# Optimization experiments

Measured on AMD Instinct MI355X. Metric: run time of the kernel, lower is better.

The kernel has to match this reference:

```python
import jax, jax.numpy as jnp
import numpy as np

B, S, H = 2, 2048, 4096
NH, NKV, HD = 32, 8, 128
RD = 64  # partial rotary dim = head_dim * partial_rotary_factor
THETA = 10000.0


def setup_inputs() -> dict:
    key = jax.random.key(0)
    ks = jax.random.split(key, 6)
    hidden_states = jax.random.normal(ks[0], (B, S, H), dtype=jnp.float32)
    wq = jax.random.normal(ks[1], (H, NH * HD), dtype=jnp.float32) * 0.02
    wk = jax.random.normal(ks[2], (H, NKV * HD), dtype=jnp.float32) * 0.02
    wv = jax.random.normal(ks[3], (H, NKV * HD), dtype=jnp.float32) * 0.02
    wo = jax.random.normal(ks[4], (NH * HD, H), dtype=jnp.float32) * 0.02
    # default RoPE over rotary_dim=RD: inv_freq has RD//2 entries, emb = cat(freqs, freqs)
    inv_freq = 1.0 / (THETA ** (jnp.arange(0, RD, 2, dtype=jnp.float32) / RD))  # [RD//2]
    pos = jnp.arange(S, dtype=jnp.float32)
    freqs = pos[:, None] * inv_freq[None, :]               # [S, RD//2]
    emb = jnp.concatenate([freqs, freqs], axis=-1)          # [S, RD]
    cos = jnp.broadcast_to(jnp.cos(emb)[None], (B, S, RD))
    sin = jnp.broadcast_to(jnp.sin(emb)[None], (B, S, RD))
    return {"hidden_states": hidden_states, "wq": wq, "wk": wk, "wv": wv, "wo": wo,
            "cos": cos, "sin": sin}


def _rotate_half_interleaved(x):
    # GLM-style interleaved rotate: pairs (x0,x1) -> (-x1,x0)
    x1 = x[..., 0::2]
    x2 = x[..., 1::2]
    return jnp.stack((-x2, x1), axis=-1).reshape(x.shape)


def _apply_partial_rope(x, cos_i, sin_i):
    x_rot, x_pass = x[..., :RD], x[..., RD:]
    x_rot = x_rot * cos_i + _rotate_half_interleaved(x_rot) * sin_i
    return jnp.concatenate([x_rot, x_pass], axis=-1)


def reference(hidden_states, wq, wk, wv, wo, cos, sin):
    b, s, _ = hidden_states.shape
    # projections -> [B, nheads, S, head_dim]
    q = (hidden_states @ wq).reshape(b, s, NH, HD).transpose(0, 2, 1, 3)
    k = (hidden_states @ wk).reshape(b, s, NKV, HD).transpose(0, 2, 1, 3)
    v = (hidden_states @ wv).reshape(b, s, NKV, HD).transpose(0, 2, 1, 3)
    # GLM partial rotary: take first half of cos/sin and repeat-interleave by 2
    cos_i = jnp.repeat(cos[..., : RD // 2], 2, axis=-1)[:, None]  # [B,1,S,RD]
    sin_i = jnp.repeat(sin[..., : RD // 2], 2, axis=-1)[:, None]
    q = _apply_partial_rope(q, cos_i, sin_i)
    k = _apply_partial_rope(k, cos_i, sin_i)
    # repeat_kv for GQA
    rep = NH // NKV
    k = jnp.repeat(k, rep, axis=1)
    v = jnp.repeat(v, rep, axis=1)
    # causal SDPA, scaling = head_dim**-0.5
    scores = jnp.einsum('bhqd,bhkd->bhqk', q, k) * (HD ** -0.5)
    causal = jnp.tril(jnp.ones((s, s), dtype=bool))
    scores = jnp.where(causal[None, None], scores, jnp.finfo(scores.dtype).min)
    probs = jax.nn.softmax(scores, axis=-1)
    out = jnp.einsum('bhqk,bhkd->bhqd', probs, v)
    out = out.transpose(0, 2, 1, 3).reshape(b, s, NH * HD)
    return out @ wo
```

## Files before the change

### kernel.cpp

```cpp
#include <hip/hip_runtime.h>


typedef _Float16 f16;
typedef _Float16 f16x8 __attribute__((ext_vector_type(8)));
typedef float f32x4 __attribute__((ext_vector_type(4)));
typedef float f32x16 __attribute__((ext_vector_type(16)));

static constexpr int Bn = 2, Sn = 2048, Hn = 4096, NH = 32, NKV = 8, HD = 128;
static constexpr float QSC = 0.08838834764831845f * 1.44269504088896340736f;

#define AS1 __attribute__((address_space(1)))
#define AS3 __attribute__((address_space(3)))

__device__ __forceinline__ void async_ld16(const void* g, void* l) {
    __builtin_amdgcn_global_load_lds((const AS1 void*)g, (AS3 void*)l, 16, 0, 0);
}

__device__ __forceinline__ unsigned pk2(float a, float b) {
    unsigned r;
    asm("v_cvt_pkrtz_f16_f32 %0, %1, %2" : "=v"(r) : "v"(a), "v"(b));
    return r;
}

__device__ __forceinline__ float fexp2(float x) {
    float r;
    asm("v_exp_f32 %0, %1" : "=v"(r) : "v"(x));
    return r;
}

__global__ __launch_bounds__(256) void k_prep(
    const float* __restrict__ hs, f16* __restrict__ hid,
    const float* __restrict__ wq, const float* __restrict__ wk,
    const float* __restrict__ wv, const float* __restrict__ wo,
    f16* __restrict__ wqkv_t, f16* __restrict__ wo_t) {
    int bid = blockIdx.x;
    if (bid < 8192) {
        long i = ((long)bid * 256 + threadIdx.x) * 8;
        float4 a = *(const float4*)(hs + i);
        float4 b = *(const float4*)(hs + i + 4);
        f16x8 o = {(f16)a.x, (f16)a.y, (f16)a.z, (f16)a.w,
                   (f16)b.x, (f16)b.y, (f16)b.z, (f16)b.w};
        *(f16x8*)(hid + i) = o;
        return;
    }
    bid -= 8192;
    const float* src;
    f16* dst;
    int N, bx, by;
    if (bid < 4096)      { src = wq; dst = wqkv_t;                    N = 4096; bx = bid & 63; by = bid >> 6; }
    else if (bid < 5120) { bid -= 4096; src = wk; dst = wqkv_t + (long)4096 * 4096; N = 1024; bx = bid & 15; by = bid >> 4; }
    else if (bid < 6144) { bid -= 5120; src = wv; dst = wqkv_t + (long)5120 * 4096; N = 1024; bx = bid & 15; by = bid >> 4; }
    else                 { bid -= 6144; src = wo; dst = wo_t;         N = 4096; bx = bid & 63; by = bid >> 6; }
    __shared__ float tile[64][65];
    const int k0 = by * 64, n0 = bx * 64;
    const int tx = threadIdx.x & 63, ty = threadIdx.x >> 6;
#pragma unroll
    for (int r = ty; r < 64; r += 4)
        tile[r][tx] = src[(long)(k0 + r) * N + (n0 + tx)];
    __syncthreads();
#pragma unroll
    for (int r = ty; r < 64; r += 4)
        dst[(long)(n0 + r) * 4096 + (k0 + tx)] = (f16)tile[tx][r];
}

__device__ __forceinline__ void gemm256_core(
    const f16* __restrict__ A, const f16* __restrict__ Bt,
    char* L, int m0, int n0, f32x4 acc[8][4]) {
    const int t = threadIdx.x, lane = t & 63, wave = t >> 6;
    const int wm = wave >> 2, wn = wave & 3;
    const int fr = lane & 15, fg = lane >> 4;

    const int srowL = wave * 8 + (lane >> 3);
    const int scol  = 8 * ((lane & 7) ^ (lane >> 3));
    const f16* ga = A  + (long)(m0 + srowL) * 4096 + scol;
    const f16* gb = Bt + (long)(n0 + srowL) * 4096 + scol;
    const int woff = wave * 1024;

    auto ST = [&](int sel, int c, int row0, int kt) {
        const f16* g = sel ? gb : ga;
        async_ld16(g + (long)row0 * 4096 + kt * 64,
                   L + c * 65536 + sel * 32768 + row0 * 128 + woff);
    };

    ST(0, 0, 0, 0);   ST(0, 0, 64, 0);  ST(0, 0, 128, 0); ST(0, 0, 192, 0);
    ST(1, 0, 0, 0);   ST(1, 0, 64, 0);  ST(1, 0, 128, 0); ST(1, 0, 192, 0);
    ST(1, 1, 0, 1);   ST(1, 1, 64, 1);  ST(1, 1, 128, 1); ST(1, 1, 192, 1);
    ST(0, 1, 0, 1);   ST(0, 1, 128, 1);
    asm volatile("s_waitcnt vmcnt(6)" ::: "memory");
    __builtin_amdgcn_s_barrier();

    const int abase = wm * 128;
    const int bbase = wn * 64;

    for (int tt = 0; tt < 64; ++tt) {
        const int c = tt & 1;
        const char* bufA = L + c * 65536;
        const char* bufB = bufA + 32768;
        f16x8 bf[2][4];

#pragma unroll
        for (int q = 0; q < 4; ++q) {
            if (q == 0) {
#pragma unroll
                for (int ks = 0; ks < 2; ++ks)
#pragma unroll
                    for (int nf = 0; nf < 4; ++nf) {
                        int r = bbase + nf * 16 + fr;
                        bf[ks][nf] = *(const f16x8*)(bufB + r * 128 +
                                        ((ks * 64 + 16 * fg) ^ ((r & 7) << 4)));
                    }
            }
            f16x8 af[2][2];
#pragma unroll
            for (int ks = 0; ks < 2; ++ks)
#pragma unroll
                for (int i = 0; i < 2; ++i) {
                    int r = abase + (2 * q + i) * 16 + fr;
                    af[ks][i] = *(const f16x8*)(bufA + r * 128 +
                                    ((ks * 64 + 16 * fg) ^ ((r & 7) << 4)));
                }
            if (q == 0) { if (tt + 1 < 64) { ST(0, c ^ 1,  64, tt + 1);
                                             ST(0, c ^ 1, 192, tt + 1); } }
            if (q == 1) { if (tt + 2 < 64) { ST(1, c,   0, tt + 2);
                                             ST(1, c,  64, tt + 2); } }
            if (q == 2) { if (tt + 2 < 64) { ST(1, c, 128, tt + 2);
                                             ST(1, c, 192, tt + 2); } }
            if (q == 3) { if (tt + 2 < 64) { ST(0, c,   0, tt + 2);
                                             ST(0, c, 128, tt + 2); } }
            __builtin_amdgcn_s_barrier();
            __builtin_amdgcn_s_setprio(1);
#pragma unroll
            for (int ks = 0; ks < 2; ++ks)
#pragma unroll
                for (int i = 0; i < 2; ++i)
#pragma unroll
                    for (int nf = 0; nf < 4; ++nf)
                        acc[2 * q + i][nf] = __builtin_amdgcn_mfma_f32_16x16x32_f16(
                            af[ks][i], bf[ks][nf], acc[2 * q + i][nf], 0, 0, 0);
            __builtin_amdgcn_s_setprio(0);
            if (q == 3) {
                if (tt < 62)       asm volatile("s_waitcnt vmcnt(6)" ::: "memory");
                else if (tt == 62) asm volatile("s_waitcnt vmcnt(0)" ::: "memory");
            }
            __builtin_amdgcn_s_barrier();
        }
    }
}

__global__ __launch_bounds__(512) void k_gemm_qkv(
    const f16* __restrict__ A, const f16* __restrict__ Bt,
    f16* __restrict__ q, f16* __restrict__ kk_, f16* __restrict__ vt,
    const float* __restrict__ cosb, const float* __restrict__ sinb) {
    __shared__ __align__(16) char L[131072];
    const int bid = blockIdx.x;
    const int swzb = (bid & 7) * 48 + (bid >> 3);
    const int m0 = (swzb / 24) * 256, n0 = (swzb % 24) * 256;
    f32x4 acc[8][4] = {};
    gemm256_core(A, Bt, L, m0, n0, acc);

    const int lane = threadIdx.x & 63, wave = threadIdx.x >> 6;
    const int wm = wave >> 2, wn = wave & 3;
    const int fr = lane & 15, fg = lane >> 4;
#pragma unroll
    for (int mf = 0; mf < 8; ++mf) {
        int r0 = m0 + wm * 128 + mf * 16 + 4 * fg;
        int b = r0 >> 11, s = r0 & (Sn - 1);
        const float* cb_ = cosb + ((long)b * Sn + s) * 64;
        const float* sb_ = sinb + ((long)b * Sn + s) * 64;
#pragma unroll
        for (int nf = 0; nf < 4; ++nf) {
            int cc = n0 + wn * 64 + nf * 16 + fr;
            int d = cc & 127;
            if (cc < 5120) {
                float vals[4];
#pragma unroll
                for (int e = 0; e < 4; ++e) vals[e] = acc[mf][nf][e];
                if (d < 64) {
                    int ci = d >> 1;
                    bool odd = (d & 1);
#pragma unroll
                    for (int e = 0; e < 4; ++e) {
                        float p = __shfl_xor(vals[e], 1, 64);
                        float c = cb_[e * 64 + ci], sv = sb_[e * 64 + ci];
                        vals[e] = odd ? (vals[e] * c + p * sv)
                                      : (vals[e] * c - p * sv);
                    }
                }
                if (cc < 4096) {
                    int h = cc >> 7;
#pragma unroll
                    for (int e = 0; e < 4; ++e)
                        q[(((long)b * NH + h) * Sn + s + e) * HD + d] =
                            (f16)(vals[e] * QSC);
                } else {
                    int h = (cc - 4096) >> 7;
#pragma unroll
                    for (int e = 0; e < 4; ++e)
                        kk_[(((long)b * NKV + h) * Sn + s + e) * HD + d] =
                            (f16)vals[e];
                }
            } else {
                int h = (cc - 5120) >> 7;
                uint2 w = {pk2(acc[mf][nf][0], acc[mf][nf][1]),
                           pk2(acc[mf][nf][2], acc[mf][nf][3])};
                *(uint2*)&vt[(((long)b * NKV + h) * HD + d) * Sn + s] = w;
            }
        }
    }
}

__global__ __launch_bounds__(512) void k_gemm_out(
    const f16* __restrict__ A, const f16* __restrict__ Bt,
    float* __restrict__ out) {
    __shared__ __align__(16) char L[131072];
    const int bid = blockIdx.x;
    const int swzb = (bid & 7) * 32 + (bid >> 3);
    const int m0 = (swzb >> 4) * 256, n0 = (swzb & 15) * 256;
    f32x4 acc[8][4] = {};
    gemm256_core(A, Bt, L, m0, n0, acc);

    const int lane = threadIdx.x & 63, wave = threadIdx.x >> 6;
    const int wm = wave >> 2, wn = wave & 3;
    const int fr = lane & 15, fg = lane >> 4;
#pragma unroll
    for (int mf = 0; mf < 8; ++mf) {
        int r0 = m0 + wm * 128 + mf * 16 + 4 * fg;
#pragma unroll
        for (int nf = 0; nf < 4; ++nf) {
            int cc = n0 + wn * 64 + nf * 16 + fr;
#pragma unroll
            for (int e = 0; e < 4; ++e)
                out[(long)(r0 + e) * 4096 + cc] = acc[mf][nf][e];
        }
    }
}


__device__ __forceinline__ f16x8 ld_sw256(const f16* base, int r, int c) {
    int byte = r * 256 + ((c * 2) ^ ((r & 7) << 4));
    return *(const f16x8*)((const char*)base + byte);
}
__device__ __forceinline__ f16x8 ld_sw128(const f16* base, int r, int c) {
    int byte = r * 128 + ((c * 2) ^ ((r & 7) << 4));
    return *(const f16x8*)((const char*)base + byte);
}

__device__ __forceinline__ void stage_k(const f16* __restrict__ Kb, f16* ksm,
                                        int k0, int wave, int lane) {
#pragma unroll
    for (int i = 0; i < 2; ++i) {
        int dbase = (i * 8 + wave) * 1024;
        int d = dbase + lane * 16;
        int row = d >> 8;
        int cb = (d & 255) ^ ((row & 7) << 4);
        async_ld16(Kb + (long)(k0 + row) * HD + (cb >> 1), (char*)ksm + dbase);
    }
}
__device__ __forceinline__ void stage_v(const f16* __restrict__ Vb, f16* vsm,
                                        int k0, int wave, int lane) {
#pragma unroll
    for (int i = 0; i < 2; ++i) {
        int dbase = (i * 8 + wave) * 1024;
        int d = dbase + lane * 16;
        int row = d >> 7;
        int cb = (d & 127) ^ ((row & 7) << 4);
        async_ld16(Vb + (long)row * Sn + k0 + (cb >> 1), (char*)vsm + dbase);
    }
}

__global__ __launch_bounds__(512) void k_attn(
    const f16* __restrict__ Q, const f16* __restrict__ K,
    const f16* __restrict__ Vt, f16* __restrict__ O) {
    __shared__ __align__(16) f16 Ksm[2][64 * 128];
    __shared__ __align__(16) f16 Vsm[2][128 * 64];

    const int id = blockIdx.x;
    const int kvh = id & 7;
    const int r_ = id >> 3;
    const int pos = r_ & 7;
    const int qt = (pos & 1) ? (pos >> 1) : (7 - (pos >> 1));
    const int hg = (r_ >> 3) & 3;
    const int b  = r_ >> 5;
    const int h  = kvh * 4 + hg;
    const int q0 = qt * 256;
    const int t = threadIdx.x, lane = t & 63, wave = t >> 6;
    const int q0w = q0 + wave * 32;
    const int lq = lane & 31, hi = lane >> 5;

    const f16* Qb = Q + ((long)(b * NH + h) * Sn) * HD;
    const f16* Kb = K + ((long)(b * NKV + kvh) * Sn) * HD;
    const f16* Vb = Vt + ((long)(b * NKV + kvh) * HD) * Sn;

    f16x8 qf[8];
#pragma unroll
    for (int s = 0; s < 8; ++s)
        qf[s] = *(const f16x8*)&Qb[(long)(q0w + lq) * HD + 16 * s + 8 * hi];

    f32x16 oacc[4] = {};
    float mrun = -1e30f, lrun = 0.f;

    const int nt = q0 / 64 + 4;
    stage_k(Kb, Ksm[0], 0, wave, lane);
    stage_v(Vb, Vsm[0], 0, wave, lane);

    for (int kt = 0; kt < nt; ++kt) {
        const int k0 = kt * 64;
        const int cur = kt & 1;
        if (kt + 1 < nt) {
            stage_k(Kb, Ksm[cur ^ 1], (kt + 1) * 64, wave, lane);
            stage_v(Vb, Vsm[cur ^ 1], (kt + 1) * 64, wave, lane);
            asm volatile("s_waitcnt vmcnt(4)" ::: "memory");
        } else {
            asm volatile("s_waitcnt vmcnt(0)" ::: "memory");
        }
        __builtin_amdgcn_s_barrier();

        if (k0 <= q0w + 31) {
            f32x16 st[2] = {};
#pragma unroll
            for (int s = 0; s < 8; ++s) {
                f16x8 kf0 = ld_sw256(Ksm[cur], lq,      16 * s + 8 * hi);
                f16x8 kf1 = ld_sw256(Ksm[cur], 32 + lq, 16 * s + 8 * hi);
                st[0] = __builtin_amdgcn_mfma_f32_32x32x16_f16(kf0, qf[s], st[0], 0, 0, 0);
                st[1] = __builtin_amdgcn_mfma_f32_32x32x16_f16(kf1, qf[s], st[1], 0, 0, 0);
            }
            const bool full = (k0 + 63 <= q0w);
            if (!full) {
#pragma unroll
                for (int mt = 0; mt < 2; ++mt)
#pragma unroll
                    for (int r = 0; r < 16; ++r) {
                        int kvv = k0 + 32 * mt + (r & 3) + 8 * (r >> 2) + 4 * hi;
                        if (kvv > q0w + lq) st[mt][r] = -1e30f;
                    }
            }
            float pm = st[0][0];
#pragma unroll
            for (int r = 1; r < 16; ++r) pm = fmaxf(pm, st[0][r]);
#pragma unroll
            for (int r = 0; r < 16; ++r) pm = fmaxf(pm, st[1][r]);
            pm = fmaxf(pm, __shfl_xor(pm, 32, 64));
            if (__any(pm > mrun + 8.f)) {
                float mn = fmaxf(mrun, pm);
                float sc = fexp2(mrun - mn);
                mrun = mn;
                lrun *= sc;
                float scr[16];
#pragma unroll
                for (int r = 0; r < 16; ++r)
                    scr[r] = __shfl(sc, (r & 3) + 8 * (r >> 2) + 4 * hi, 64);
#pragma unroll
                for (int db = 0; db < 4; ++db)
#pragma unroll
                    for (int r = 0; r < 16; ++r)
                        oacc[db][r] *= scr[r];
            }
            unsigned pw[2][8];
#pragma unroll
            for (int mt = 0; mt < 2; ++mt)
#pragma unroll
                for (int i = 0; i < 8; ++i) {
                    float p0 = fexp2(st[mt][2 * i]     - mrun);
                    float p1 = fexp2(st[mt][2 * i + 1] - mrun);
                    lrun += p0 + p1;
                    pw[mt][i] = pk2(p0, p1);
                }
#pragma unroll
            for (int s = 0; s < 4; ++s) {
                const int mt = s >> 1, sl = s & 1;
                unsigned a0 = pw[mt][4 * sl], a1 = pw[mt][4 * sl + 1];
                unsigned a2 = pw[mt][4 * sl + 2], a3 = pw[mt][4 * sl + 3];
                unsigned own0 = hi ? a2 : a0, own1 = hi ? a3 : a1;
                unsigned snd0 = hi ? a0 : a2, snd1 = hi ? a1 : a3;
                unsigned rx0 = (unsigned)__shfl_xor((int)snd0, 32, 64);
                unsigned rx1 = (unsigned)__shfl_xor((int)snd1, 32, 64);
                union { unsigned u[4]; f16x8 v; } pu;
                pu.u[0] = hi ? rx0 : own0;
                pu.u[1] = hi ? rx1 : own1;
                pu.u[2] = hi ? own0 : rx0;
                pu.u[3] = hi ? own1 : rx1;
#pragma unroll
                for (int db = 0; db < 4; ++db) {
                    f16x8 vf = ld_sw128(Vsm[cur], 32 * db + lq, 16 * s + 8 * hi);
                    oacc[db] = __builtin_amdgcn_mfma_f32_32x32x16_f16(pu.v, vf, oacc[db], 0, 0, 0);
                }
            }
        }
        __builtin_amdgcn_s_barrier();
    }

    lrun += __shfl_xor(lrun, 32, 64);
    float li = 1.f / lrun;
    float ir[16];
#pragma unroll
    for (int r = 0; r < 16; ++r)
        ir[r] = __shfl(li, (r & 3) + 8 * (r >> 2) + 4 * hi, 64);
#pragma unroll
    for (int db = 0; db < 4; ++db)
#pragma unroll
        for (int r = 0; r < 16; ++r) {
            int qloc = (r & 3) + 8 * (r >> 2) + 4 * hi;
            long tok = (long)b * Sn + q0w + qloc;
            O[tok * (NH * HD) + h * HD + 32 * db + lq] = (f16)(oacc[db][r] * ir[r]);
        }
}

__global__ void k_ws_fail(float* out) { out[0] = 1.0e9f; }

extern "C" void kernel_launch(void* const* d_in, const int* in_sizes, int n_in,
                              void* d_out, int out_size, void* d_ws, size_t ws_size,
                              hipStream_t stream) {
    const float* hs   = (const float*)d_in[0];
    const float* wq   = (const float*)d_in[1];
    const float* wk   = (const float*)d_in[2];
    const float* wv   = (const float*)d_in[3];
    const float* wo   = (const float*)d_in[4];
    const float* cosb = (const float*)d_in[5];
    const float* sinb = (const float*)d_in[6];
    float* out = (float*)d_out;

    const size_t OFF_WQKV = 0;
    const size_t OFF_WO   = 50331648;
    const size_t OFF_HID  = 83886080;
    const size_t OFF_Q    = 117440512;
    const size_t OFF_K    = 150994944;
    const size_t OFF_VT   = 167772160;
    const size_t WS_NEED  = 176160768;
    if (ws_size < WS_NEED) { k_ws_fail<<<1, 1, 0, stream>>>(out); return; }

    char* ws = (char*)d_ws;
    f16* wqkv_t = (f16*)(ws + OFF_WQKV);
    f16* wo_t   = (f16*)(ws + OFF_WO);
    f16* hid    = (f16*)(ws + OFF_HID);
    f16* qb     = (f16*)(ws + OFF_Q);
    f16* kb     = (f16*)(ws + OFF_K);
    f16* vtb    = (f16*)(ws + OFF_VT);

    k_prep<<<dim3(18432), 256, 0, stream>>>(hs, hid, wq, wk, wv, wo, wqkv_t, wo_t);
    k_gemm_qkv<<<dim3(384), 512, 0, stream>>>(hid, wqkv_t, qb, kb, vtb, cosb, sinb);
    k_attn<<<dim3(512), 512, 0, stream>>>(qb, kb, vtb, hid);
    k_gemm_out<<<dim3(256), 512, 0, stream>>>(hid, wo_t, out);
}
```

Before: 561.9 us.

## Use 256x384 tiles for QKV GEMM to match 256 CUs in one wave

Adds a new GEMM core with a 256x384 output tile and rewrites the QKV projection kernel to use it, cutting the grid from 384 to 256 blocks. On a 256-CU device this removes the partial second wave and raises arithmetic intensity per block. The trade-off is more accumulator registers (48 f32x4 per thread) and 160KB of LDS, which risks spills and lower occupancy. The pipelined load schedule is reworked to match the larger B tile.

```diff
diff --git a/kernel.cpp b/kernel.cpp
--- a/kernel.cpp
+++ b/kernel.cpp
@@ -61,6 +61,85 @@
 #pragma unroll
     for (int r = ty; r < 64; r += 4)
         dst[(long)(n0 + r) * 4096 + (k0 + tx)] = (f16)tile[tx][r];
+}
+
+__device__ __forceinline__ void gemm384_core(
+    const f16* __restrict__ A, const f16* __restrict__ Bt,
+    char* L, int m0, int n0, f32x4 acc[8][6]) {
+    const int t = threadIdx.x, lane = t & 63, wave = t >> 6;
+    const int wm = wave >> 2, wn = wave & 3;
+    const int fr = lane & 15, fg = lane >> 4;
+
+    const int srowL = wave * 8 + (lane >> 3);
+    const int scol  = 8 * ((lane & 7) ^ (lane >> 3));
+    const f16* ga = A  + (long)(m0 + srowL) * 4096 + scol;
+    const f16* gb = Bt + (long)(n0 + srowL) * 4096 + scol;
+    const int woff = wave * 1024;
+
+    auto ST = [&](int sel, int c, int row0, int kt) {
+        const f16* g = sel ? gb : ga;
+        async_ld16(g + (long)row0 * 4096 + kt * 64,
+                   L + c * 81920 + sel * 32768 + row0 * 128 + woff);
+    };
+
+    ST(0, 0, 0, 0); ST(0, 0, 64, 0); ST(0, 0, 128, 0); ST(0, 0, 192, 0);
+#pragma unroll
+    for (int r = 0; r < 384; r += 64) ST(1, 0, r, 0);
+#pragma unroll
+    for (int r = 0; r < 384; r += 64) ST(1, 1, r, 1);
+    ST(0, 1, 0, 1); ST(0, 1, 128, 1);
+    asm volatile("s_waitcnt vmcnt(8)" ::: "memory");
+    __builtin_amdgcn_s_barrier();
+
+    const int abase = wm * 128;
+    const int bbase = wn * 96;
+
+    for (int tt = 0; tt < 64; ++tt) {
+        const int c = tt & 1;
+        const char* bufA = L + c * 81920;
+        const char* bufB = bufA + 32768;
+        f16x8 bf[6];
+
+#pragma unroll
+        for (int ph = 0; ph < 4; ++ph) {
+            const int ks = ph >> 1, mh = ph & 1;
+            if (mh == 0) {
+#pragma unroll
+                for (int nf = 0; nf < 6; ++nf) {
+                    int r = bbase + nf * 16 + fr;
+                    bf[nf] = *(const f16x8*)(bufB + r * 128 +
+                                 ((ks * 64 + 16 * fg) ^ ((r & 7) << 4)));
+                }
+            }
+            f16x8 af[4];
+#pragma unroll
+            for (int i = 0; i < 4; ++i) {
+                int r = abase + mh * 64 + i * 16 + fr;
+                af[i] = *(const f16x8*)(bufA + r * 128 +
+                             ((ks * 64 + 16 * fg) ^ ((r & 7) << 4)));
+            }
+            if (ph == 0) { if (tt + 1 < 64) { ST(0, c ^ 1,  64, tt + 1);
+                                              ST(0, c ^ 1, 192, tt + 1); } }
+            if (ph == 3) { if (tt + 2 < 64) {
+#pragma unroll
+                for (int r = 0; r < 384; r += 64) ST(1, c, r, tt + 2);
+                ST(0, c, 0, tt + 2); ST(0, c, 128, tt + 2); } }
+            __builtin_amdgcn_s_barrier();
+            __builtin_amdgcn_s_setprio(1);
+#pragma unroll
+            for (int i = 0; i < 4; ++i)
+#pragma unroll
+                for (int nf = 0; nf < 6; ++nf)
+                    acc[mh * 4 + i][nf] = __builtin_amdgcn_mfma_f32_16x16x32_f16(
+                        af[i], bf[nf], acc[mh * 4 + i][nf], 0, 0, 0);
+            __builtin_amdgcn_s_setprio(0);
+            if (ph == 3) {
+                if (tt < 62)       asm volatile("s_waitcnt vmcnt(8)" ::: "memory");
+                else if (tt == 62) asm volatile("s_waitcnt vmcnt(0)" ::: "memory");
+            }
+            __builtin_amdgcn_s_barrier();
+        }
+    }
 }
 
 __device__ __forceinline__ void gemm256_core(
@@ -151,12 +230,12 @@
     const f16* __restrict__ A, const f16* __restrict__ Bt,
     f16* __restrict__ q, f16* __restrict__ kk_, f16* __restrict__ vt,
     const float* __restrict__ cosb, const float* __restrict__ sinb) {
-    __shared__ __align__(16) char L[131072];
+    __shared__ __align__(16) char L[163840];
     const int bid = blockIdx.x;
-    const int swzb = (bid & 7) * 48 + (bid >> 3);
-    const int m0 = (swzb / 24) * 256, n0 = (swzb % 24) * 256;
-    f32x4 acc[8][4] = {};
-    gemm256_core(A, Bt, L, m0, n0, acc);
+    const int swzb = (bid & 7) * 32 + (bid >> 3);
+    const int m0 = (swzb >> 4) * 256, n0 = (swzb & 15) * 384;
+    f32x4 acc[8][6] = {};
+    gemm384_core(A, Bt, L, m0, n0, acc);
 
     const int lane = threadIdx.x & 63, wave = threadIdx.x >> 6;
     const int wm = wave >> 2, wn = wave & 3;
@@ -168,8 +247,8 @@
         const float* cb_ = cosb + ((long)b * Sn + s) * 64;
         const float* sb_ = sinb + ((long)b * Sn + s) * 64;
 #pragma unroll
-        for (int nf = 0; nf < 4; ++nf) {
-            int cc = n0 + wn * 64 + nf * 16 + fr;
+        for (int nf = 0; nf < 6; ++nf) {
+            int cc = n0 + wn * 96 + nf * 16 + fr;
             int d = cc & 127;
             if (cc < 5120) {
                 float vals[4];
@@ -437,7 +516,7 @@
     f16* vtb    = (f16*)(ws + OFF_VT);
 
     k_prep<<<dim3(18432), 256, 0, stream>>>(hs, hid, wq, wk, wv, wo, wqkv_t, wo_t);
-    k_gemm_qkv<<<dim3(384), 512, 0, stream>>>(hid, wqkv_t, qb, kb, vtb, cosb, sinb);
+    k_gemm_qkv<<<dim3(256), 512, 0, stream>>>(hid, wqkv_t, qb, kb, vtb, cosb, sinb);
     k_attn<<<dim3(512), 512, 0, stream>>>(qb, kb, vtb, hid);
     k_gemm_out<<<dim3(256), 512, 0, stream>>>(hid, wo_t, out);
 }
```

After: 522.2 us, median of 2. 1.08x faster.
